# Kernel optimization log

Measured on AMD Instinct MI355X. Metric: run time of the kernel, lower is better.

## Reference

```python
import jax, jax.numpy as jnp
import numpy as np

DATA_DIM = 10000
ID_EMBED_DIM = 256
QK_DIM = 64
B, N = 4, 4096
SCALE = QK_DIM ** (-0.5)


def setup_inputs() -> dict:
    key = jax.random.key(0)
    k1, k2, k3, k4, k5, k6, k7 = jax.random.split(key, 7)
    val = jax.random.normal(k1, (B, N), dtype=jnp.float32)
    pos = jax.random.randint(k2, (B, N), 0, DATA_DIM + 1)
    # learned params (torch default inits approximated with scaled normals/uniforms)
    embed = jax.random.normal(k3, (DATA_DIM + 1, ID_EMBED_DIM), dtype=jnp.float32)
    lim = 1.0 / np.sqrt(ID_EMBED_DIM)
    Wq = jax.random.uniform(k4, (QK_DIM, ID_EMBED_DIM), minval=-lim, maxval=lim, dtype=jnp.float32)
    bq = jax.random.uniform(k5, (QK_DIM,), minval=-lim, maxval=lim, dtype=jnp.float32)
    Wk = jax.random.uniform(k6, (QK_DIM, ID_EMBED_DIM), minval=-lim, maxval=lim, dtype=jnp.float32)
    bk = jax.random.uniform(k7, (QK_DIM,), minval=-lim, maxval=lim, dtype=jnp.float32)
    return {"t": 0, "val": val, "pos": pos, "embed": embed,
            "Wq": Wq, "bq": bq, "Wk": Wk, "bk": bk}


def reference(t, val, pos, embed, Wq, bq, Wk, bk):
    # t is unused (ODE-style signature)
    id_embed = embed[pos]                              # [B, N, E] gather
    q = jnp.einsum('bne,de->bnd', id_embed, Wq) + bq   # [B, N, D]
    k = jnp.einsum('bne,de->bnd', id_embed, Wk) + bk   # [B, N, D]
    # soft_weights[b,i,j] = q[b,i,:] . k[b,j,:] * scale  (no softmax)
    soft_weights = jnp.einsum('bid,bjd->bij', q, k) * SCALE  # [B, N, N]
    fx = jnp.einsum('bij,bi->bj', soft_weights, val)         # contract over i
    return val + val * fx
```

## Files before the change

kernel.cpp:

```cpp
#include <hip/hip_runtime.h>

#define NN 4096
#define BB 4
#define EE 256
#define DD 64
#define SCALE 0.125f

#define ROWS1 32
__global__ void k_accum(const float* __restrict__ val, const int* __restrict__ pos,
                        const float* __restrict__ embed,
                        float* __restrict__ u, float* __restrict__ Vsum) {
    const int b = blockIdx.y;
    const int e = threadIdx.x;
    const int base = blockIdx.x * ROWS1;
    float acc = 0.f;
    float vsum = 0.f;
    #pragma unroll 4
    for (int r = 0; r < ROWS1; ++r) {
        const int i = base + r;
        const float v = val[b * NN + i];
        const int p = pos[b * NN + i];
        acc += v * embed[(size_t)p * EE + e];
        vsum += v;
    }
    atomicAdd(&u[b * EE + e], acc);
    if (e == 0) atomicAdd(&Vsum[b], vsum);
}

__global__ void k_small(const float* __restrict__ u, const float* __restrict__ Vsum,
                        const float* __restrict__ Wq, const float* __restrict__ bq,
                        const float* __restrict__ Wk, const float* __restrict__ bk,
                        float* __restrict__ w, float* __restrict__ c) {
    const int b = blockIdx.x;
    const int t = threadIdx.x;
    __shared__ float sS[DD];
    if (t < DD) {
        float acc = bq[t] * Vsum[b];
        const float* uu = u + b * EE;
        const float* wq = Wq + t * EE;
        #pragma unroll 4
        for (int e = 0; e < EE; ++e) acc += uu[e] * wq[e];
        sS[t] = acc;
    }
    __syncthreads();
    float acc = 0.f;
    #pragma unroll 8
    for (int d = 0; d < DD; ++d) acc += sS[d] * Wk[d * EE + t];
    w[b * EE + t] = acc;
    if (t == 0) {
        float cc = 0.f;
        for (int d = 0; d < DD; ++d) cc += sS[d] * bk[d];
        c[b] = cc;
    }
}

#define ROWS3 4
__global__ void k_out(const float* __restrict__ val, const int* __restrict__ pos,
                      const float* __restrict__ embed,
                      const float* __restrict__ w, const float* __restrict__ c,
                      float* __restrict__ out) {
    const int b = blockIdx.y;
    const int lane = threadIdx.x & 63;
    const int wv = threadIdx.x >> 6;
    const int j0 = (blockIdx.x * 4 + wv) * ROWS3;
    const float4 wf = reinterpret_cast<const float4*>(w + b * EE)[lane];
    const float cb = c[b];
    #pragma unroll
    for (int r = 0; r < ROWS3; ++r) {
        const int j = j0 + r;
        const int p = pos[b * NN + j];
        const float4 ev = reinterpret_cast<const float4*>(embed + (size_t)p * EE)[lane];
        float acc = ev.x * wf.x + ev.y * wf.y + ev.z * wf.z + ev.w * wf.w;
        #pragma unroll
        for (int off = 32; off > 0; off >>= 1) acc += __shfl_down(acc, off, 64);
        if (lane == 0) {
            const float fx = SCALE * (acc + cb);
            const float v = val[b * NN + j];
            out[b * NN + j] = v * (1.f + fx);
        }
    }
}

extern "C" void kernel_launch(void* const* d_in, const int* in_sizes, int n_in,
                              void* d_out, int out_size, void* d_ws, size_t ws_size,
                              hipStream_t stream) {
    const float* val   = (const float*)d_in[1];
    const int*   pos   = (const int*)d_in[2];
    const float* embed = (const float*)d_in[3];
    const float* Wq    = (const float*)d_in[4];
    const float* bq    = (const float*)d_in[5];
    const float* Wk    = (const float*)d_in[6];
    const float* bk    = (const float*)d_in[7];
    float* out = (float*)d_out;

    float* ws = (float*)d_ws;
    float* u  = ws;
    float* V  = ws + BB * EE;
    float* w  = ws + BB * EE + BB;
    float* c  = ws + 2 * BB * EE + BB;

    hipMemsetAsync(u, 0, (BB * EE + BB) * sizeof(float), stream);

    dim3 g1(NN / ROWS1, BB);
    k_accum<<<g1, 256, 0, stream>>>(val, pos, embed, u, V);

    k_small<<<BB, 256, 0, stream>>>(u, V, Wq, bq, Wk, bk, w, c);

    dim3 g3(NN / (4 * ROWS3), BB);
    k_out<<<g3, 256, 0, stream>>>(val, pos, embed, w, c, out);
}
```

Baseline: 105.1 us.

## Fuse projection kernel into output kernel and vectorize gather accumulation

Removes the tiny k_small launch by having every block of the output kernel recompute the Wq/Wk projections of the accumulated vector in shared memory before its gather-dot loop. The accumulation kernel now reads embedding rows with float4 loads, one wave per row, and reduces the four waves in shared memory, so it issues fewer atomics per block. The output kernel handles more rows per wave. Every block now repeats the small matvec, reading Wq and Wk (about 128 KB) again, in exchange for one fewer launch and its serialization.

```diff
diff --git a/kernel.cpp b/kernel.cpp
--- a/kernel.cpp
+++ b/kernel.cpp
@@ -6,67 +6,96 @@
 #define DD 64
 #define SCALE 0.125f
 
-#define ROWS1 32
-__global__ void k_accum(const float* __restrict__ val, const int* __restrict__ pos,
-                        const float* __restrict__ embed,
-                        float* __restrict__ u, float* __restrict__ Vsum) {
-    const int b = blockIdx.y;
-    const int e = threadIdx.x;
-    const int base = blockIdx.x * ROWS1;
-    float acc = 0.f;
+#define RW1 16
+#define RB1 (4 * RW1)
+__global__ __launch_bounds__(256) void k_accum(
+        const float* __restrict__ val, const int* __restrict__ pos,
+        const float* __restrict__ embed,
+        float* __restrict__ u, float* __restrict__ Vsum) {
+    const int b    = blockIdx.y;
+    const int t    = threadIdx.x;
+    const int lane = t & 63;
+    const int wv   = t >> 6;
+    const int base = blockIdx.x * RB1 + wv * RW1;
+
+    float4 acc = make_float4(0.f, 0.f, 0.f, 0.f);
     float vsum = 0.f;
     #pragma unroll 4
-    for (int r = 0; r < ROWS1; ++r) {
+    for (int r = 0; r < RW1; ++r) {
         const int i = base + r;
         const float v = val[b * NN + i];
-        const int p = pos[b * NN + i];
-        acc += v * embed[(size_t)p * EE + e];
+        const int   p = pos[b * NN + i];
+        const float4 ev = reinterpret_cast<const float4*>(embed + (size_t)p * EE)[lane];
+        acc.x += v * ev.x; acc.y += v * ev.y;
+        acc.z += v * ev.z; acc.w += v * ev.w;
         vsum += v;
     }
-    atomicAdd(&u[b * EE + e], acc);
-    if (e == 0) atomicAdd(&Vsum[b], vsum);
+
+    __shared__ float part[4][EE];
+    __shared__ float vpart[4];
+    *reinterpret_cast<float4*>(&part[wv][lane * 4]) = acc;
+    if (lane == 0) vpart[wv] = vsum;
+    __syncthreads();
+
+    const float s = part[0][t] + part[1][t] + part[2][t] + part[3][t];
+    atomicAdd(&u[b * EE + t], s);
+    if (t == 0) atomicAdd(&Vsum[b], vpart[0] + vpart[1] + vpart[2] + vpart[3]);
 }
 
-__global__ void k_small(const float* __restrict__ u, const float* __restrict__ Vsum,
-                        const float* __restrict__ Wq, const float* __restrict__ bq,
-                        const float* __restrict__ Wk, const float* __restrict__ bk,
-                        float* __restrict__ w, float* __restrict__ c) {
-    const int b = blockIdx.x;
-    const int t = threadIdx.x;
+#define RW2 16
+#define RB2 (4 * RW2)
+__global__ __launch_bounds__(256) void k_fused(
+        const float* __restrict__ val, const int* __restrict__ pos,
+        const float* __restrict__ embed,
+        const float* __restrict__ u, const float* __restrict__ Vsum,
+        const float* __restrict__ Wq, const float* __restrict__ bq,
+        const float* __restrict__ Wk, const float* __restrict__ bk,
+        float* __restrict__ out) {
+    const int b    = blockIdx.y;
+    const int t    = threadIdx.x;
+    const int lane = t & 63;
+    const int wv   = t >> 6;
+
+    __shared__ float ps[4][DD];
     __shared__ float sS[DD];
-    if (t < DD) {
-        float acc = bq[t] * Vsum[b];
-        const float* uu = u + b * EE;
-        const float* wq = Wq + t * EE;
-        #pragma unroll 4
-        for (int e = 0; e < EE; ++e) acc += uu[e] * wq[e];
-        sS[t] = acc;
+    __shared__ float wsh[EE];
+    __shared__ float cSh;
+
+    {
+        const int d = t & 63, seg = t >> 6;
+        const float4* uu = reinterpret_cast<const float4*>(u + b * EE + seg * 64);
+        const float4* wq = reinterpret_cast<const float4*>(Wq + (size_t)d * EE + seg * 64);
+        float acc = 0.f;
+        #pragma unroll
+        for (int q = 0; q < 16; ++q) {
+            const float4 a = uu[q], w4 = wq[q];
+            acc += a.x * w4.x + a.y * w4.y + a.z * w4.z + a.w * w4.w;
+        }
+        ps[seg][d] = acc;
     }
     __syncthreads();
-    float acc = 0.f;
-    #pragma unroll 8
-    for (int d = 0; d < DD; ++d) acc += sS[d] * Wk[d * EE + t];
-    w[b * EE + t] = acc;
-    if (t == 0) {
-        float cc = 0.f;
-        for (int d = 0; d < DD; ++d) cc += sS[d] * bk[d];
-        c[b] = cc;
+    if (t < DD) sS[t] = ps[0][t] + ps[1][t] + ps[2][t] + ps[3][t] + bq[t] * Vsum[b];
+    __syncthreads();
+
+    if (wv == 0) {
+        float x = sS[lane] * bk[lane];
+        #pragma unroll
+        for (int off = 32; off > 0; off >>= 1) x += __shfl_down(x, off, 64);
+        if (lane == 0) cSh = x;
     }
-}
+    {
+        float acc = 0.f;
+        #pragma unroll
+        for (int d = 0; d < DD; ++d) acc += sS[d] * Wk[d * EE + t];
+        wsh[t] = acc;
+    }
+    __syncthreads();
 
-#define ROWS3 4
-__global__ void k_out(const float* __restrict__ val, const int* __restrict__ pos,
-                      const float* __restrict__ embed,
-                      const float* __restrict__ w, const float* __restrict__ c,
-                      float* __restrict__ out) {
-    const int b = blockIdx.y;
-    const int lane = threadIdx.x & 63;
-    const int wv = threadIdx.x >> 6;
-    const int j0 = (blockIdx.x * 4 + wv) * ROWS3;
-    const float4 wf = reinterpret_cast<const float4*>(w + b * EE)[lane];
-    const float cb = c[b];
-    #pragma unroll
-    for (int r = 0; r < ROWS3; ++r) {
+    const float4 wf = reinterpret_cast<const float4*>(wsh)[lane];
+    const float  cb = cSh;
+    const int j0 = blockIdx.x * RB2 + wv * RW2;
+    #pragma unroll 4
+    for (int r = 0; r < RW2; ++r) {
         const int j = j0 + r;
         const int p = pos[b * NN + j];
         const float4 ev = reinterpret_cast<const float4*>(embed + (size_t)p * EE)[lane];
@@ -74,9 +103,8 @@
         #pragma unroll
         for (int off = 32; off > 0; off >>= 1) acc += __shfl_down(acc, off, 64);
         if (lane == 0) {
-            const float fx = SCALE * (acc + cb);
             const float v = val[b * NN + j];
-            out[b * NN + j] = v * (1.f + fx);
+            out[b * NN + j] = v * (1.f + SCALE * (acc + cb));
         }
     }
 }
@@ -96,16 +124,12 @@
     float* ws = (float*)d_ws;
     float* u  = ws;
     float* V  = ws + BB * EE;
-    float* w  = ws + BB * EE + BB;
-    float* c  = ws + 2 * BB * EE + BB;
 
     hipMemsetAsync(u, 0, (BB * EE + BB) * sizeof(float), stream);
 
-    dim3 g1(NN / ROWS1, BB);
+    dim3 g1(NN / RB1, BB);
     k_accum<<<g1, 256, 0, stream>>>(val, pos, embed, u, V);
 
-    k_small<<<BB, 256, 0, stream>>>(u, V, Wq, bq, Wk, bk, w, c);
-
-    dim3 g3(NN / (4 * ROWS3), BB);
-    k_out<<<g3, 256, 0, stream>>>(val, pos, embed, w, c, out);
+    dim3 g2(NN / RB2, BB);
+    k_fused<<<g2, 256, 0, stream>>>(val, pos, embed, u, V, Wq, bq, Wk, bk, out);
 }
```

After: 94.88 us. -9.7%, faster.
